# Kernel optimization log

Measured on AMD Instinct MI355X. Metric: run time of the kernel, lower is better.

Reference implementation:

```python
import jax, jax.numpy as jnp
import numpy as np

# --- cfg constants (from init_kwargs) ---
T = 100
DT_MS = 1.0
MAX_RATE_HZ = 200.0
TAU_MEM = 20.0
TAU_PRE = 20.0
TAU_POST = 20.0
V_TH = 16.0
LR_POST = 0.01
LR_PRE = 0.012
W_MAX = 1.0
B, F, N_IN = 256, 1024, 784


def setup_inputs() -> dict:
    key = jax.random.key(0)
    k1, k2, k3 = jax.random.split(key, 3)
    image = jax.random.uniform(k1, (B, 1, 28, 28), dtype=jnp.float32)
    noise = jax.random.uniform(k2, (T, B, 1, 28, 28), dtype=jnp.float32)
    # non-negative excitatory weights, kernel 28x28 flattened -> (F, 784)
    W = jax.random.uniform(k3, (F, N_IN), dtype=jnp.float32) * 0.3
    return {"image": image, "W": W, "noise": noise}


def reference(image, W, noise):
    """Returns spike_count: (B, n_filters)."""
    b = image.shape[0]
    f = W.shape[0]
    # Poisson encoding: P(spike at t) = rate*dt = image * max_rate_hz * dt_ms/1000
    p = image.reshape(b, -1) * (MAX_RATE_HZ * DT_MS / 1000.0)        # (B, 784)
    spikes_in = (noise.reshape(T, b, -1) < p[None]).astype(jnp.float32)  # (T, B, 784)

    decay_mem = jnp.float32(np.exp(-DT_MS / TAU_MEM))
    decay_pre = jnp.float32(np.exp(-DT_MS / TAU_PRE))
    decay_post = jnp.float32(np.exp(-DT_MS / TAU_POST))

    def step(carry, pre):
        mem, w, apre, apost, cnt = carry
        # conv with 28x28 kernel, padding 0 == FC: (B,784) @ (784,F)
        I = pre @ w.T                                   # (B, F)
        mem = mem * decay_mem + I
        spk = (mem >= V_TH).astype(mem.dtype)           # LIF threshold
        mem = mem * (1.0 - spk)                         # reset to 0 on spike
        # --- STDP (pair-based, batch-averaged, Diehl & Cook style) ---
        apre = apre * decay_pre + pre                   # (B, 784) pre trace
        dw_plus = (LR_POST / b) * jnp.einsum('bf,bi->fi', spk, apre)   # LTP on post spike
        dw_minus = (LR_PRE / b) * jnp.einsum('bf,bi->fi', apost, pre)  # LTD on pre spike
        w = jnp.clip(w + dw_plus - dw_minus, 0.0, W_MAX)
        apost = apost * decay_post + spk                # (B, F) post trace
        cnt = cnt + spk
        return (mem, w, apre, apost, cnt), None

    init = (jnp.zeros((b, f), jnp.float32),   # mem
            W,                                 # plastic weights
            jnp.zeros((b, N_IN), jnp.float32), # apre
            jnp.zeros((b, f), jnp.float32),    # apost
            jnp.zeros((b, f), jnp.float32))    # spike_count
    (mem, w, apre, apost, cnt), _ = jax.lax.scan(step, init, spikes_in)
    return cnt
```

## Files before the change

kernel.cpp:

```cpp
#include <hip/hip_runtime.h>
#include <math.h>

#define TSTEPS 100
#define BB 256
#define FF 1024
#define NIN 784
#define NW 13
#define CAPA 192
#define CAPB 128
#define NBLK 1024
#define TPB 256

typedef unsigned long long u64;

__device__ __forceinline__ unsigned at_add(unsigned* p, unsigned v) {
    return __hip_atomic_fetch_add(p, v, __ATOMIC_RELAXED, __HIP_MEMORY_SCOPE_AGENT);
}
__device__ __forceinline__ unsigned at_ld(unsigned* p) {
    return __hip_atomic_load(p, __ATOMIC_RELAXED, __HIP_MEMORY_SCOPE_AGENT);
}
__device__ __forceinline__ void at_st(unsigned* p, unsigned v) {
    __hip_atomic_store(p, v, __ATOMIC_RELAXED, __HIP_MEMORY_SCOPE_AGENT);
}
__device__ __forceinline__ u64 at_ld64(u64* p) {
    return __hip_atomic_load(p, __ATOMIC_RELAXED, __HIP_MEMORY_SCOPE_AGENT);
}
__device__ __forceinline__ void at_st64(u64* p, u64 v) {
    __hip_atomic_store(p, v, __ATOMIC_RELAXED, __HIP_MEMORY_SCOPE_AGENT);
}

__device__ __forceinline__ float sc0_ld(const float* p) {
    float v;
    asm volatile("global_load_dword %0, %1, off sc0\n\t"
                 "s_waitcnt vmcnt(0)"
                 : "=v"(v) : "v"(p) : "memory");
    __builtin_amdgcn_sched_barrier(0);
    return v;
}
__device__ __forceinline__ void sc0_ld2(const float* p0, const float* p1,
                                        float& v0, float& v1) {
    asm volatile("global_load_dword %0, %2, off sc0\n\t"
                 "global_load_dword %1, %3, off sc0\n\t"
                 "s_waitcnt vmcnt(0)"
                 : "=&v"(v0), "=&v"(v1) : "v"(p0), "v"(p1) : "memory");
    __builtin_amdgcn_sched_barrier(0);
}
__device__ __forceinline__ void sc0_ld8(
    const float* p0, const float* p1, const float* p2, const float* p3,
    const float* p4, const float* p5, const float* p6, const float* p7,
    float& v0, float& v1, float& v2, float& v3,
    float& v4, float& v5, float& v6, float& v7)
{
    asm volatile(
        "global_load_dword %0, %8, off sc0\n\t"
        "global_load_dword %1, %9, off sc0\n\t"
        "global_load_dword %2, %10, off sc0\n\t"
        "global_load_dword %3, %11, off sc0\n\t"
        "global_load_dword %4, %12, off sc0\n\t"
        "global_load_dword %5, %13, off sc0\n\t"
        "global_load_dword %6, %14, off sc0\n\t"
        "global_load_dword %7, %15, off sc0\n\t"
        "s_waitcnt vmcnt(0)"
        : "=&v"(v0),"=&v"(v1),"=&v"(v2),"=&v"(v3),
          "=&v"(v4),"=&v"(v5),"=&v"(v6),"=&v"(v7)
        : "v"(p0),"v"(p1),"v"(p2),"v"(p3),"v"(p4),"v"(p5),"v"(p6),"v"(p7)
        : "memory");
    __builtin_amdgcn_sched_barrier(0);
}

__global__ __launch_bounds__(256) void k_init(
    const float* __restrict__ W, float* __restrict__ wT,
    float* __restrict__ apreT_g, float* __restrict__ mem, float* __restrict__ apost,
    float* __restrict__ out, u64* __restrict__ spkbits, u64* __restrict__ spkT,
    unsigned* __restrict__ bar)
{
    int idx = blockIdx.x * 256 + threadIdx.x;
    {
        int f = idx & (FF - 1);
        int i = idx >> 10;
        wT[idx] = W[f * NIN + i];
    }
    apreT_g[idx] = 0.f;
    apreT_g[idx + NIN * FF] = 0.f;
    if (idx < BB * FF) { mem[idx] = 0.f; apost[idx] = 0.f; out[idx] = 0.f; }
    if (idx < BB * 16) spkbits[idx] = 0ull;
    if (idx < 2 * FF * 4) spkT[idx] = 0ull;
    if (idx < 4096) bar[idx] = 0u;
}

__global__ __launch_bounds__(256) void k_encode(
    const float* __restrict__ image, const float* __restrict__ noise,
    u64* __restrict__ prebits)
{
    int tid = blockIdx.x * 256 + threadIdx.x;
    int lane = threadIdx.x & 63;
    int word = tid >> 6;
    int wd = word % NW;
    int tb = word / NW;
    int b = tb & (BB - 1);
    int i = (wd << 6) + lane;
    bool s = false;
    if (i < NIN) {
        float pf = __fmul_rn(image[b * NIN + i], 0.2f);
        s = (noise[(size_t)tb * NIN + i] < pf);
    }
    u64 m = __ballot(s);
    if (lane == 0) prebits[word] = m;
}

__global__ __launch_bounds__(256) void k_encode_t(
    const u64* __restrict__ prebits, u64* __restrict__ prebitsT)
{
    int tid = blockIdx.x * 256 + threadIdx.x;
    int b = tid & (BB - 1);
    int ti = tid >> 8;
    int i = ti % NIN;
    int t = ti / NIN;
    u64 w = prebits[((size_t)t * BB + b) * NW + (i >> 6)];
    bool s = (w >> (i & 63)) & 1ull;
    u64 m = __ballot(s);
    if ((threadIdx.x & 63) == 0)
        prebitsT[(size_t)ti * 4 + ((threadIdx.x >> 6) & 3)] = m;
}

__global__ __launch_bounds__(256) void k_lists(
    const u64* __restrict__ prebits, unsigned short* __restrict__ idxA,
    unsigned short* __restrict__ cntA)
{
    int tb = blockIdx.x * 256 + threadIdx.x;
    const u64* pb = prebits + (size_t)tb * NW;
    unsigned short* ia = idxA + (size_t)tb * CAPA;
    int n = 0, c1 = 0, c2 = 0;
    for (int wd = 0; wd < NW; ++wd) {
        u64 m = pb[wd];
        int boff = wd << 6;
        while (m) {
            int j = __builtin_ctzll(m); m &= m - 1;
            if (n < CAPA) ia[n] = (unsigned short)(boff + j);
            ++n;
        }
        if (wd == 5)  c1 = n;
        if (wd == 11) c2 = n;
    }
    if (n > CAPA) n = CAPA;
    if (c2 > n) c2 = n;
    if (c1 > c2) c1 = c2;
    cntA[tb * 4 + 0] = (unsigned short)c1;
    cntA[tb * 4 + 1] = (unsigned short)c2;
    cntA[tb * 4 + 2] = (unsigned short)n;
}

__global__ __launch_bounds__(256) void k_listsT(
    const u64* __restrict__ prebitsT, unsigned char* __restrict__ idxB,
    unsigned short* __restrict__ cntB)
{
    int ti = blockIdx.x * 256 + threadIdx.x;
    if (ti >= TSTEPS * NIN) return;
    const u64* pt = prebitsT + (size_t)ti * 4;
    unsigned char* ib = idxB + (size_t)ti * CAPB;
    int n = 0;
    for (int wb = 0; wb < 4; ++wb) {
        u64 m = pt[wb];
        int boff = wb << 6;
        while (m) {
            int j = __builtin_ctzll(m); m &= m - 1;
            if (n < CAPB) ib[n] = (unsigned char)(boff + j);
            ++n;
        }
    }
    cntB[ti] = (unsigned short)(n > CAPB ? CAPB : n);
}

__global__ __launch_bounds__(TPB, 4) void k_run(
    float* __restrict__ wT, float* __restrict__ apreT_g, float* __restrict__ apost,
    float* __restrict__ mem,
    const u64* __restrict__ prebits,
    const unsigned short* __restrict__ idxA, const unsigned short* __restrict__ cntA,
    const unsigned char* __restrict__ idxB, const unsigned short* __restrict__ cntB,
    u64* __restrict__ spkbits, u64* __restrict__ spkT,
    float* __restrict__ out, unsigned* __restrict__ bar,
    float dmem, float dpre, float dpost, float lrp, float lrm)
{
    __shared__ int sh[4];
    __shared__ int shs[8];
    __shared__ float sap[2][256];
    const int tix = threadIdx.x;
    const int sub = tix >> 7, lane = tix & 127;

    if (tix == 0) {
        unsigned xcd;
        asm volatile("s_getreg_b32 %0, hwreg(HW_REG_XCC_ID)" : "=s"(xcd));
        xcd &= 7u;
        unsigned rank = at_add(bar + xcd * 16, 1u);
        asm volatile("s_waitcnt vmcnt(0)" ::: "memory");
        unsigned a = at_add(bar + 128, 1u);
        if (a == NBLK - 1u) at_st(bar + 136, 1u);
        unsigned spins = 0;
        while (at_ld(bar + 136) == 0u) {
            if (++spins > (1u << 24)) break;
            __builtin_amdgcn_s_sleep(2);
        }
        int cnts[8]; int Kn = 0, gidx = 0;
        for (int x = 0; x < 8; ++x) cnts[x] = (int)at_ld(bar + x * 16);
        for (int x = 0; x < 8; ++x)
            if (cnts[x] > 0) { if (x == (int)xcd) gidx = Kn; ++Kn; }
        int ns = 0;
        for (int s = 0; s < 8; ++s) if ((s % Kn) == gidx) shs[ns++] = s;
        sh[0] = (int)xcd; sh[1] = (int)rank; sh[2] = cnts[xcd]; sh[3] = ns;
    }
    __syncthreads();
    const int xcd = sh[0], rank = sh[1], nx = sh[2], nsl = sh[3];
    float* apx = apreT_g + (size_t)xcd * (BB * NIN);

    const int ukA = ((nsl << 8) + 2 * nx - 1) / (2 * nx);
    const int ukB = (nsl * NIN + 2 * nx - 1) / (2 * nx);
    unsigned ep = 1;

    for (int t = 0; t < TSTEPS; ++t) {
        u64* cur = spkT + (size_t)(t & 1) * (FF * 4);
        u64* nxt = spkT + (size_t)((t + 1) & 1) * (FF * 4);

        for (int q = 0; q < ukA; ++q) {
            int u = rank * 2 + sub + q * 2 * nx;
            if (u < (nsl << 8)) {
                int sl = u >> 8, b = u & 255;
                int f = (shs[sl] << 7) + lane;
                int tid = (b << 10) + f;

                u64 pw_ = spkbits[(b << 4) + (f >> 6)];
                float apo = __fadd_rn(__fmul_rn(apost[tid], dpost),
                                      (float)((pw_ >> (f & 63)) & 1ull));
                apost[tid] = apo;

                const unsigned short* ia = idxA + (size_t)(t * BB + b) * CAPA;
                const unsigned short* ca = cntA + (size_t)(t * BB + b) * 4;
                int c1 = ca[0], c2 = ca[1], c3 = ca[2];
                float I = 0.f;
                int k = 0;
                #pragma unroll 1
                for (int ch = 0; ch < 3; ++ch) {
                    int ke = (ch == 0) ? c1 : (ch == 1) ? c2 : c3;
                    float c = 0.f;
                    for (; k + 8 <= ke; k += 8) {
                        float v0,v1,v2,v3,v4,v5,v6,v7;
                        sc0_ld8(wT + ((int)ia[k+0] << 10) + f, wT + ((int)ia[k+1] << 10) + f,
                                wT + ((int)ia[k+2] << 10) + f, wT + ((int)ia[k+3] << 10) + f,
                                wT + ((int)ia[k+4] << 10) + f, wT + ((int)ia[k+5] << 10) + f,
                                wT + ((int)ia[k+6] << 10) + f, wT + ((int)ia[k+7] << 10) + f,
                                v0,v1,v2,v3,v4,v5,v6,v7);
                        c = __fadd_rn(c, v0); c = __fadd_rn(c, v1);
                        c = __fadd_rn(c, v2); c = __fadd_rn(c, v3);
                        c = __fadd_rn(c, v4); c = __fadd_rn(c, v5);
                        c = __fadd_rn(c, v6); c = __fadd_rn(c, v7);
                    }
                    for (; k < ke; ++k)
                        c = __fadd_rn(c, sc0_ld(wT + ((int)ia[k] << 10) + f));
                    I = __fadd_rn(I, c);
                }

                float mm = __fadd_rn(__fmul_rn(mem[tid], dmem), I);
                bool spk = (mm >= 16.0f);
                mem[tid] = spk ? 0.f : mm;
                if (spk) {
                    out[tid] += 1.f;
                    atomicOr(&cur[(f << 2) | (b >> 6)], 1ull << (b & 63));
                }
                u64 bal = __ballot(spk);
                if ((tix & 63) == 0) spkbits[(b << 4) + (f >> 6)] = bal;

                if (sl == 0) {
                    const u64* pbr = prebits + ((size_t)t * BB + b) * NW;
                    for (int i2 = lane; i2 < NIN; i2 += 128) {
                        u64 w_ = pbr[i2 >> 6];
                        float pr = (float)((w_ >> (i2 & 63)) & 1ull);
                        int ai = (i2 << 8) + b;
                        apx[ai] = __fadd_rn(__fmul_rn(apx[ai], dpre), pr);
                    }
                }
            }
        }
        for (int wd = rank * TPB + tix; wd < (nsl << 9); wd += nx * TPB)
            at_st64(&nxt[(shs[wd >> 9] << 9) + (wd & 511)], 0ull);

        if (t == TSTEPS - 1) break;

        asm volatile("s_waitcnt vmcnt(0) lgkmcnt(0)" ::: "memory");
        __syncthreads();
        if (tix == 0) {
            int nsub = nx < 16 ? nx : 16;
            int sb = rank % nsub;
            unsigned need = (unsigned)((nx - sb + nsub - 1) / nsub);
            unsigned v = at_add(bar + 256 + (xcd * 16 + sb) * 16, 1u);
            if (v == need * ep - 1u) {
                unsigned r = at_add(bar + 2560 + xcd * 16, 1u);
                if (r == (unsigned)nsub * ep - 1u) at_st(bar + 2816 + xcd * 16, ep);
            }
            unsigned spins = 0;
            while (at_ld(bar + 2816 + xcd * 16) < ep) {
                if (++spins > (1u << 24)) break;
                __builtin_amdgcn_s_sleep(2);
            }
        }
        __syncthreads();
        ++ep;

        for (int q = 0; q < ukB; ++q) {
            int u = rank * 2 + sub + q * 2 * nx;
            bool act = (u < nsl * NIN);
            int sl = act ? u / NIN : 0;
            int i = act ? (u - sl * NIN) : 0;
            int f = (shs[sl] << 7) + lane;
            float Sm = 0.f;
            u64 m0 = 0, m1 = 0, m2 = 0, m3 = 0;
            if (act) {
                const unsigned char* ib = idxB + (size_t)(t * NIN + i) * CAPB;
                int cb = cntB[t * NIN + i];
                int k = 0;
                for (; k + 8 <= cb; k += 8) {
                    float v0,v1,v2,v3,v4,v5,v6,v7;
                    sc0_ld8(apost + ((int)ib[k+0] << 10) + f, apost + ((int)ib[k+1] << 10) + f,
                            apost + ((int)ib[k+2] << 10) + f, apost + ((int)ib[k+3] << 10) + f,
                            apost + ((int)ib[k+4] << 10) + f, apost + ((int)ib[k+5] << 10) + f,
                            apost + ((int)ib[k+6] << 10) + f, apost + ((int)ib[k+7] << 10) + f,
                            v0,v1,v2,v3,v4,v5,v6,v7);
                    Sm = __fadd_rn(Sm, v0); Sm = __fadd_rn(Sm, v1);
                    Sm = __fadd_rn(Sm, v2); Sm = __fadd_rn(Sm, v3);
                    Sm = __fadd_rn(Sm, v4); Sm = __fadd_rn(Sm, v5);
                    Sm = __fadd_rn(Sm, v6); Sm = __fadd_rn(Sm, v7);
                }
                for (; k < cb; ++k)
                    Sm = __fadd_rn(Sm, sc0_ld(apost + ((int)ib[k] << 10) + f));

                float r0, r1;
                sc0_ld2(apx + (i << 8) + lane, apx + (i << 8) + 128 + lane, r0, r1);
                sap[sub][lane] = r0; sap[sub][128 + lane] = r1;

                m0 = at_ld64(&cur[(f << 2) | 0]);
                m1 = at_ld64(&cur[(f << 2) | 1]);
                m2 = at_ld64(&cur[(f << 2) | 2]);
                m3 = at_ld64(&cur[(f << 2) | 3]);
            }
            __syncthreads();
            if (act) {
                const float* sp_ = sap[sub];
                float Sp = 0.f;
                u64 m;
                m = m0; while (m) { int j = __builtin_ctzll(m); m &= m - 1;
                                    Sp = __fadd_rn(Sp, sp_[j]); }
                m = m1; while (m) { int j = __builtin_ctzll(m); m &= m - 1;
                                    Sp = __fadd_rn(Sp, sp_[64 + j]); }
                m = m2; while (m) { int j = __builtin_ctzll(m); m &= m - 1;
                                    Sp = __fadd_rn(Sp, sp_[128 + j]); }
                m = m3; while (m) { int j = __builtin_ctzll(m); m &= m - 1;
                                    Sp = __fadd_rn(Sp, sp_[192 + j]); }

                int wi = (i << 10) + f;
                float w = wT[wi];
                w = __fadd_rn(w, __fmul_rn(lrp, Sp));
                w = __fsub_rn(w, __fmul_rn(lrm, Sm));
                w = fminf(fmaxf(w, 0.f), 1.f);
                wT[wi] = w;
            }
            __syncthreads();
        }

        asm volatile("s_waitcnt vmcnt(0) lgkmcnt(0)" ::: "memory");
        __syncthreads();
        if (tix == 0) {
            int nsub = nx < 16 ? nx : 16;
            int sb = rank % nsub;
            unsigned need = (unsigned)((nx - sb + nsub - 1) / nsub);
            unsigned v = at_add(bar + 256 + (xcd * 16 + sb) * 16, 1u);
            if (v == need * ep - 1u) {
                unsigned r = at_add(bar + 2560 + xcd * 16, 1u);
                if (r == (unsigned)nsub * ep - 1u) at_st(bar + 2816 + xcd * 16, ep);
            }
            unsigned spins = 0;
            while (at_ld(bar + 2816 + xcd * 16) < ep) {
                if (++spins > (1u << 24)) break;
                __builtin_amdgcn_s_sleep(2);
            }
        }
        __syncthreads();
        ++ep;
    }
}

extern "C" void kernel_launch(void* const* d_in, const int* in_sizes, int n_in,
                              void* d_out, int out_size, void* d_ws, size_t ws_size,
                              hipStream_t stream)
{
    const float* image = (const float*)d_in[0];
    const float* W     = (const float*)d_in[1];
    const float* noise = (const float*)d_in[2];
    float* out = (float*)d_out;

    char* p = (char*)d_ws;
    float* wT      = (float*)p; p += (size_t)NIN * FF * 4;
    float* apreT_g = (float*)p; p += (size_t)8 * BB * NIN * 4;
    float* apost   = (float*)p; p += (size_t)BB * FF * 4;
    float* mem     = (float*)p; p += (size_t)BB * FF * 4;
    u64* prebits   = (u64*)p;   p += (size_t)TSTEPS * BB * NW * 8;
    u64* prebitsT  = (u64*)p;   p += (size_t)TSTEPS * NIN * 4 * 8;
    u64* spkbits   = (u64*)p;   p += (size_t)BB * 16 * 8;
    u64* spkT      = (u64*)p;   p += (size_t)2 * FF * 4 * 8;
    unsigned short* idxA = (unsigned short*)p; p += (size_t)TSTEPS * BB * CAPA * 2;
    unsigned short* cntA = (unsigned short*)p; p += (size_t)TSTEPS * BB * 4 * 2;
    unsigned char*  idxB = (unsigned char*)p;  p += (size_t)TSTEPS * NIN * CAPB;
    unsigned short* cntB = (unsigned short*)p; p += (size_t)TSTEPS * NIN * 2;
    unsigned* bar        = (unsigned*)p;       p += 4096 * 4;

    float dmem = (float)exp(-1.0 / 20.0);
    float dpre = dmem, dpost = dmem;
    float lrp = (float)(0.01 / 256.0);
    float lrm = (float)(0.012 / 256.0);

    k_init<<<(NIN * FF) / 256, 256, 0, stream>>>(
        W, wT, apreT_g, mem, apost, out, spkbits, spkT, bar);
    k_encode<<<(TSTEPS * BB * NW * 64) / 256, 256, 0, stream>>>(image, noise, prebits);
    k_encode_t<<<(TSTEPS * NIN * BB) / 256, 256, 0, stream>>>(prebits, prebitsT);
    k_lists<<<(TSTEPS * BB) / 256, 256, 0, stream>>>(prebits, idxA, cntA);
    k_listsT<<<(TSTEPS * NIN + 255) / 256, 256, 0, stream>>>(prebitsT, idxB, cntB);

    k_run<<<NBLK, TPB, 0, stream>>>(
        wT, apreT_g, apost, mem, prebits, idxA, cntA, idxB, cntB,
        spkbits, spkT, out, bar, dmem, dpre, dpost, lrp, lrm);
}
```

Baseline: 5.928 ms.

## Restructure persistent kernel to per-wave work units with register state and flag barrier

Reworks the persistent STDP kernel. Each wave of 64 lanes now owns a feature slice instead of each half-block of 128, membrane, count and post-trace state stay in registers across timesteps rather than round-tripping global memory, and gather loads are issued 16 at a time before a single wait. The pre-trace update is vectorized over a transposed layout, and the old atomic counter tree barrier is replaced by a per-XCD arrive/release flag barrier led by rank 0. Startup rank discovery moves to a slot table. The changes aim to cut global traffic, memory latency stalls and barrier cost, at the price of more registers per thread and more complex synchronisation.

```diff
diff --git a/kernel.cpp b/kernel.cpp
--- a/kernel.cpp
+++ b/kernel.cpp
@@ -10,12 +10,11 @@
 #define CAPB 128
 #define NBLK 1024
 #define TPB 256
+#define BARSZ 17408
 
 typedef unsigned long long u64;
-
-__device__ __forceinline__ unsigned at_add(unsigned* p, unsigned v) {
-    return __hip_atomic_fetch_add(p, v, __ATOMIC_RELAXED, __HIP_MEMORY_SCOPE_AGENT);
-}
+typedef float f4 __attribute__((ext_vector_type(4)));
+
 __device__ __forceinline__ unsigned at_ld(unsigned* p) {
     return __hip_atomic_load(p, __ATOMIC_RELAXED, __HIP_MEMORY_SCOPE_AGENT);
 }
@@ -37,15 +36,15 @@
     __builtin_amdgcn_sched_barrier(0);
     return v;
 }
-__device__ __forceinline__ void sc0_ld2(const float* p0, const float* p1,
-                                        float& v0, float& v1) {
-    asm volatile("global_load_dword %0, %2, off sc0\n\t"
-                 "global_load_dword %1, %3, off sc0\n\t"
+__device__ __forceinline__ f4 sc0_ld4(const f4* p) {
+    f4 v;
+    asm volatile("global_load_dwordx4 %0, %1, off sc0\n\t"
                  "s_waitcnt vmcnt(0)"
-                 : "=&v"(v0), "=&v"(v1) : "v"(p0), "v"(p1) : "memory");
+                 : "=v"(v) : "v"(p) : "memory");
     __builtin_amdgcn_sched_barrier(0);
-}
-__device__ __forceinline__ void sc0_ld8(
+    return v;
+}
+__device__ __forceinline__ void sc0_issue8(
     const float* p0, const float* p1, const float* p2, const float* p3,
     const float* p4, const float* p5, const float* p6, const float* p7,
     float& v0, float& v1, float& v2, float& v3,
@@ -59,19 +58,68 @@
         "global_load_dword %4, %12, off sc0\n\t"
         "global_load_dword %5, %13, off sc0\n\t"
         "global_load_dword %6, %14, off sc0\n\t"
-        "global_load_dword %7, %15, off sc0\n\t"
-        "s_waitcnt vmcnt(0)"
+        "global_load_dword %7, %15, off sc0"
         : "=&v"(v0),"=&v"(v1),"=&v"(v2),"=&v"(v3),
           "=&v"(v4),"=&v"(v5),"=&v"(v6),"=&v"(v7)
         : "v"(p0),"v"(p1),"v"(p2),"v"(p3),"v"(p4),"v"(p5),"v"(p6),"v"(p7)
         : "memory");
+}
+__device__ __forceinline__ void sc0_ld8(
+    const float* p0, const float* p1, const float* p2, const float* p3,
+    const float* p4, const float* p5, const float* p6, const float* p7,
+    float& v0, float& v1, float& v2, float& v3,
+    float& v4, float& v5, float& v6, float& v7)
+{
+    sc0_issue8(p0,p1,p2,p3,p4,p5,p6,p7, v0,v1,v2,v3,v4,v5,v6,v7);
+    asm volatile("s_waitcnt vmcnt(0)" ::: "memory");
     __builtin_amdgcn_sched_barrier(0);
+}
+
+template <typename IDX>
+__device__ __forceinline__ float foldList(
+    const float* __restrict__ base, const IDX* __restrict__ list,
+    int k0, int k1, int f)
+{
+    float c = 0.f;
+    int k = k0;
+    for (; k + 16 <= k1; k += 16) {
+        float v0,v1,v2,v3,v4,v5,v6,v7,v8,v9,v10,v11,v12,v13,v14,v15;
+        sc0_issue8(base+((int)list[k+0]<<10)+f, base+((int)list[k+1]<<10)+f,
+                   base+((int)list[k+2]<<10)+f, base+((int)list[k+3]<<10)+f,
+                   base+((int)list[k+4]<<10)+f, base+((int)list[k+5]<<10)+f,
+                   base+((int)list[k+6]<<10)+f, base+((int)list[k+7]<<10)+f,
+                   v0,v1,v2,v3,v4,v5,v6,v7);
+        sc0_issue8(base+((int)list[k+8]<<10)+f,  base+((int)list[k+9]<<10)+f,
+                   base+((int)list[k+10]<<10)+f, base+((int)list[k+11]<<10)+f,
+                   base+((int)list[k+12]<<10)+f, base+((int)list[k+13]<<10)+f,
+                   base+((int)list[k+14]<<10)+f, base+((int)list[k+15]<<10)+f,
+                   v8,v9,v10,v11,v12,v13,v14,v15);
+        asm volatile("s_waitcnt vmcnt(0)" ::: "memory");
+        __builtin_amdgcn_sched_barrier(0);
+        c=__fadd_rn(c,v0);  c=__fadd_rn(c,v1);  c=__fadd_rn(c,v2);  c=__fadd_rn(c,v3);
+        c=__fadd_rn(c,v4);  c=__fadd_rn(c,v5);  c=__fadd_rn(c,v6);  c=__fadd_rn(c,v7);
+        c=__fadd_rn(c,v8);  c=__fadd_rn(c,v9);  c=__fadd_rn(c,v10); c=__fadd_rn(c,v11);
+        c=__fadd_rn(c,v12); c=__fadd_rn(c,v13); c=__fadd_rn(c,v14); c=__fadd_rn(c,v15);
+    }
+    if (k + 8 <= k1) {
+        float v0,v1,v2,v3,v4,v5,v6,v7;
+        sc0_ld8(base+((int)list[k+0]<<10)+f, base+((int)list[k+1]<<10)+f,
+                base+((int)list[k+2]<<10)+f, base+((int)list[k+3]<<10)+f,
+                base+((int)list[k+4]<<10)+f, base+((int)list[k+5]<<10)+f,
+                base+((int)list[k+6]<<10)+f, base+((int)list[k+7]<<10)+f,
+                v0,v1,v2,v3,v4,v5,v6,v7);
+        c=__fadd_rn(c,v0); c=__fadd_rn(c,v1); c=__fadd_rn(c,v2); c=__fadd_rn(c,v3);
+        c=__fadd_rn(c,v4); c=__fadd_rn(c,v5); c=__fadd_rn(c,v6); c=__fadd_rn(c,v7);
+        k += 8;
+    }
+    for (; k < k1; ++k)
+        c = __fadd_rn(c, sc0_ld(base + ((int)list[k] << 10) + f));
+    return c;
 }
 
 __global__ __launch_bounds__(256) void k_init(
     const float* __restrict__ W, float* __restrict__ wT,
-    float* __restrict__ apreT_g, float* __restrict__ mem, float* __restrict__ apost,
-    float* __restrict__ out, u64* __restrict__ spkbits, u64* __restrict__ spkT,
+    float* __restrict__ apreT_g, u64* __restrict__ spkT,
     unsigned* __restrict__ bar)
 {
     int idx = blockIdx.x * 256 + threadIdx.x;
@@ -82,10 +130,8 @@
     }
     apreT_g[idx] = 0.f;
     apreT_g[idx + NIN * FF] = 0.f;
-    if (idx < BB * FF) { mem[idx] = 0.f; apost[idx] = 0.f; out[idx] = 0.f; }
-    if (idx < BB * 16) spkbits[idx] = 0ull;
     if (idx < 2 * FF * 4) spkT[idx] = 0ull;
-    if (idx < 4096) bar[idx] = 0u;
+    if (idx < BARSZ) bar[idx] = 0u;
 }
 
 __global__ __launch_bounds__(256) void k_encode(
@@ -173,217 +219,228 @@
 
 __global__ __launch_bounds__(TPB, 4) void k_run(
     float* __restrict__ wT, float* __restrict__ apreT_g, float* __restrict__ apost,
-    float* __restrict__ mem,
-    const u64* __restrict__ prebits,
     const unsigned short* __restrict__ idxA, const unsigned short* __restrict__ cntA,
     const unsigned char* __restrict__ idxB, const unsigned short* __restrict__ cntB,
-    u64* __restrict__ spkbits, u64* __restrict__ spkT,
+    const u64* __restrict__ prebitsT, u64* __restrict__ spkT,
     float* __restrict__ out, unsigned* __restrict__ bar,
     float dmem, float dpre, float dpost, float lrp, float lrm)
 {
-    __shared__ int sh[4];
-    __shared__ int shs[8];
-    __shared__ float sap[2][256];
+    __shared__ int shs[16];
+    __shared__ int shinfo[4];
+    __shared__ unsigned scnt[9];
+    __shared__ int sbad;
+    __shared__ float sap[4][256];
+
     const int tix = threadIdx.x;
-    const int sub = tix >> 7, lane = tix & 127;
-
+    const int wv = tix >> 6, lane = tix & 63;
+    const int bid = blockIdx.x;
+
+    unsigned* slot = bar;
+    if (tix < 9) scnt[tix] = 0u;
     if (tix == 0) {
-        unsigned xcd;
-        asm volatile("s_getreg_b32 %0, hwreg(HW_REG_XCC_ID)" : "=s"(xcd));
-        xcd &= 7u;
-        unsigned rank = at_add(bar + xcd * 16, 1u);
-        asm volatile("s_waitcnt vmcnt(0)" ::: "memory");
-        unsigned a = at_add(bar + 128, 1u);
-        if (a == NBLK - 1u) at_st(bar + 136, 1u);
-        unsigned spins = 0;
-        while (at_ld(bar + 136) == 0u) {
-            if (++spins > (1u << 24)) break;
-            __builtin_amdgcn_s_sleep(2);
-        }
-        int cnts[8]; int Kn = 0, gidx = 0;
-        for (int x = 0; x < 8; ++x) cnts[x] = (int)at_ld(bar + x * 16);
-        for (int x = 0; x < 8; ++x)
-            if (cnts[x] > 0) { if (x == (int)xcd) gidx = Kn; ++Kn; }
-        int ns = 0;
-        for (int s = 0; s < 8; ++s) if ((s % Kn) == gidx) shs[ns++] = s;
-        sh[0] = (int)xcd; sh[1] = (int)rank; sh[2] = cnts[xcd]; sh[3] = ns;
+        unsigned x;
+        asm volatile("s_getreg_b32 %0, hwreg(HW_REG_XCC_ID)" : "=s"(x));
+        shinfo[0] = (int)(x & 7u);
+        at_st(&slot[bid], (x & 7u) + 1u);
     }
     __syncthreads();
-    const int xcd = sh[0], rank = sh[1], nx = sh[2], nsl = sh[3];
+    const int xcd = shinfo[0];
+    unsigned mv0, mv1, mv2, mv3;
+    for (int rounds = 0;; ++rounds) {
+        if (tix == 0) sbad = 0;
+        __syncthreads();
+        mv0 = at_ld(&slot[tix]);
+        mv1 = at_ld(&slot[256 + tix]);
+        mv2 = at_ld(&slot[512 + tix]);
+        mv3 = at_ld(&slot[768 + tix]);
+        if (!(mv0 && mv1 && mv2 && mv3)) sbad = 1;
+        __syncthreads();
+        if (!sbad || rounds > (1 << 20)) break;
+        __builtin_amdgcn_s_sleep(2);
+    }
+    {
+        atomicAdd(&scnt[mv0 - 1u], 1u);
+        atomicAdd(&scnt[mv1 - 1u], 1u);
+        atomicAdd(&scnt[mv2 - 1u], 1u);
+        atomicAdd(&scnt[mv3 - 1u], 1u);
+        unsigned r = 0;
+        if ((int)(mv0 - 1u) == xcd && tix < bid) r++;
+        if ((int)(mv1 - 1u) == xcd && 256 + tix < bid) r++;
+        if ((int)(mv2 - 1u) == xcd && 512 + tix < bid) r++;
+        if ((int)(mv3 - 1u) == xcd && 768 + tix < bid) r++;
+        if (r) atomicAdd(&scnt[8], r);
+        __syncthreads();
+        if (tix == 0) {
+            int Kn = 0, gidx = 0;
+            for (int x2 = 0; x2 < 8; ++x2)
+                if (scnt[x2] > 0) { if (x2 == xcd) gidx = Kn; ++Kn; }
+            int ns = 0;
+            for (int s = 0; s < 16; ++s)
+                if ((s % Kn) == gidx) shs[ns++] = s;
+            shinfo[1] = (int)scnt[8];
+            shinfo[2] = (int)scnt[xcd];
+            shinfo[3] = ns;
+        }
+        __syncthreads();
+    }
+    const int rank = shinfo[1], nx = shinfo[2], nsl = shinfo[3];
+    const int nxw = nx * 4;
+    const int wrank = rank * 4 + wv;
+    const int nA = nsl << 8;
+    const int nB = nsl * NIN;
     float* apx = apreT_g + (size_t)xcd * (BB * NIN);
-
-    const int ukA = ((nsl << 8) + 2 * nx - 1) / (2 * nx);
-    const int ukB = (nsl * NIN + 2 * nx - 1) / (2 * nx);
+    float* sapw = sap[wv];
+    unsigned* arrive  = bar + 1024 + xcd * 1024;
+    unsigned* release = bar + 9216 + xcd * 1024;
     unsigned ep = 1;
+
+#define A_STATE(Q) float memv##Q = 0.f, cntv##Q = 0.f, apov##Q = 0.f; u64 pbal##Q = 0ull;
+    A_STATE(0) A_STATE(1) A_STATE(2) A_STATE(3)
+
+#define DO_A(Q) do { \
+    int u = wrank + (Q) * nxw; \
+    if (u < nA) { \
+        int sl = u >> 8, b = u & 255; \
+        int f = (shs[sl] << 6) + lane; \
+        apov##Q = __fadd_rn(__fmul_rn(apov##Q, dpost), \
+                            (float)((pbal##Q >> lane) & 1ull)); \
+        apost[(b << 10) + f] = apov##Q; \
+        const unsigned short* ia = idxA + (size_t)(t * BB + b) * CAPA; \
+        const unsigned short* ca = cntA + (size_t)(t * BB + b) * 4; \
+        int c1 = ca[0], c2 = ca[1], c3 = ca[2]; \
+        float I = 0.f; \
+        I = __fadd_rn(I, foldList(wT, ia, 0,  c1, f)); \
+        I = __fadd_rn(I, foldList(wT, ia, c1, c2, f)); \
+        I = __fadd_rn(I, foldList(wT, ia, c2, c3, f)); \
+        float mm = __fadd_rn(__fmul_rn(memv##Q, dmem), I); \
+        bool spk = (mm >= 16.0f); \
+        memv##Q = spk ? 0.f : mm; \
+        if (spk) { \
+            cntv##Q += 1.f; \
+            atomicOr(&cur[(f << 2) | (b >> 6)], 1ull << (b & 63)); \
+        } \
+        pbal##Q = __ballot(spk); \
+    } \
+} while (0)
+
+    auto xbar = [&]() {
+        asm volatile("s_waitcnt vmcnt(0) lgkmcnt(0)" ::: "memory");
+        __syncthreads();
+        if (rank == 0) {
+            for (int rounds = 0;; ++rounds) {
+                if (tix == 0) sbad = 0;
+                __syncthreads();
+                bool ok = true;
+                #pragma unroll
+                for (int kk = 0; kk < 4; ++kk) {
+                    int r = kk * 256 + tix;
+                    if (r < nx && r > 0) ok &= (at_ld(&arrive[r]) >= ep);
+                }
+                if (!ok) sbad = 1;
+                __syncthreads();
+                if (!sbad || rounds > (1 << 20)) break;
+                __builtin_amdgcn_s_sleep(4);
+            }
+            #pragma unroll
+            for (int kk = 0; kk < 4; ++kk) {
+                int r = kk * 256 + tix;
+                if (r < nx) at_st(&release[r], ep);
+            }
+        } else {
+            if (tix == 0) {
+                at_st(&arrive[rank], ep);
+                unsigned spins = 0;
+                while (at_ld(&release[rank]) < ep) {
+                    if (++spins > (1u << 22)) break;
+                    __builtin_amdgcn_s_sleep(8);
+                }
+            }
+            __syncthreads();
+        }
+        ++ep;
+    };
 
     for (int t = 0; t < TSTEPS; ++t) {
         u64* cur = spkT + (size_t)(t & 1) * (FF * 4);
         u64* nxt = spkT + (size_t)((t + 1) & 1) * (FF * 4);
 
-        for (int q = 0; q < ukA; ++q) {
-            int u = rank * 2 + sub + q * 2 * nx;
-            if (u < (nsl << 8)) {
-                int sl = u >> 8, b = u & 255;
-                int f = (shs[sl] << 7) + lane;
-                int tid = (b << 10) + f;
-
-                u64 pw_ = spkbits[(b << 4) + (f >> 6)];
-                float apo = __fadd_rn(__fmul_rn(apost[tid], dpost),
-                                      (float)((pw_ >> (f & 63)) & 1ull));
-                apost[tid] = apo;
-
-                const unsigned short* ia = idxA + (size_t)(t * BB + b) * CAPA;
-                const unsigned short* ca = cntA + (size_t)(t * BB + b) * 4;
-                int c1 = ca[0], c2 = ca[1], c3 = ca[2];
-                float I = 0.f;
-                int k = 0;
-                #pragma unroll 1
-                for (int ch = 0; ch < 3; ++ch) {
-                    int ke = (ch == 0) ? c1 : (ch == 1) ? c2 : c3;
-                    float c = 0.f;
-                    for (; k + 8 <= ke; k += 8) {
-                        float v0,v1,v2,v3,v4,v5,v6,v7;
-                        sc0_ld8(wT + ((int)ia[k+0] << 10) + f, wT + ((int)ia[k+1] << 10) + f,
-                                wT + ((int)ia[k+2] << 10) + f, wT + ((int)ia[k+3] << 10) + f,
-                                wT + ((int)ia[k+4] << 10) + f, wT + ((int)ia[k+5] << 10) + f,
-                                wT + ((int)ia[k+6] << 10) + f, wT + ((int)ia[k+7] << 10) + f,
-                                v0,v1,v2,v3,v4,v5,v6,v7);
-                        c = __fadd_rn(c, v0); c = __fadd_rn(c, v1);
-                        c = __fadd_rn(c, v2); c = __fadd_rn(c, v3);
-                        c = __fadd_rn(c, v4); c = __fadd_rn(c, v5);
-                        c = __fadd_rn(c, v6); c = __fadd_rn(c, v7);
-                    }
-                    for (; k < ke; ++k)
-                        c = __fadd_rn(c, sc0_ld(wT + ((int)ia[k] << 10) + f));
-                    I = __fadd_rn(I, c);
-                }
-
-                float mm = __fadd_rn(__fmul_rn(mem[tid], dmem), I);
-                bool spk = (mm >= 16.0f);
-                mem[tid] = spk ? 0.f : mm;
-                if (spk) {
-                    out[tid] += 1.f;
-                    atomicOr(&cur[(f << 2) | (b >> 6)], 1ull << (b & 63));
-                }
-                u64 bal = __ballot(spk);
-                if ((tix & 63) == 0) spkbits[(b << 4) + (f >> 6)] = bal;
-
-                if (sl == 0) {
-                    const u64* pbr = prebits + ((size_t)t * BB + b) * NW;
-                    for (int i2 = lane; i2 < NIN; i2 += 128) {
-                        u64 w_ = pbr[i2 >> 6];
-                        float pr = (float)((w_ >> (i2 & 63)) & 1ull);
-                        int ai = (i2 << 8) + b;
-                        apx[ai] = __fadd_rn(__fmul_rn(apx[ai], dpre), pr);
-                    }
-                }
-            }
-        }
-        for (int wd = rank * TPB + tix; wd < (nsl << 9); wd += nx * TPB)
-            at_st64(&nxt[(shs[wd >> 9] << 9) + (wd & 511)], 0ull);
+        DO_A(0); DO_A(1); DO_A(2); DO_A(3);
+
+        for (int r = wrank; r < NIN; r += nxw) {
+            const u64* pt = prebitsT + ((size_t)t * NIN + r) * 4;
+            u64 w0 = pt[0], w1 = pt[1], w2 = pt[2], w3 = pt[3];
+            int bb = lane << 2;
+            u64 wsel = (bb & 128) ? ((bb & 64) ? w3 : w2)
+                                  : ((bb & 64) ? w1 : w0);
+            int s0 = bb & 63;
+            f4* vp = (f4*)(apx + ((size_t)r << 8) + bb);
+            f4 v = *vp;
+            v.x = __fadd_rn(__fmul_rn(v.x, dpre), (float)((wsel >> s0) & 1ull));
+            v.y = __fadd_rn(__fmul_rn(v.y, dpre), (float)((wsel >> (s0+1)) & 1ull));
+            v.z = __fadd_rn(__fmul_rn(v.z, dpre), (float)((wsel >> (s0+2)) & 1ull));
+            v.w = __fadd_rn(__fmul_rn(v.w, dpre), (float)((wsel >> (s0+3)) & 1ull));
+            *vp = v;
+        }
+        for (int wd0 = rank * TPB + tix; wd0 < (nsl << 8); wd0 += nx * TPB) {
+            int sl = wd0 >> 8, rest = wd0 & 255;
+            int f = (shs[sl] << 6) + (rest >> 2);
+            at_st64(&nxt[(f << 2) + (rest & 3)], 0ull);
+        }
 
         if (t == TSTEPS - 1) break;
-
-        asm volatile("s_waitcnt vmcnt(0) lgkmcnt(0)" ::: "memory");
-        __syncthreads();
-        if (tix == 0) {
-            int nsub = nx < 16 ? nx : 16;
-            int sb = rank % nsub;
-            unsigned need = (unsigned)((nx - sb + nsub - 1) / nsub);
-            unsigned v = at_add(bar + 256 + (xcd * 16 + sb) * 16, 1u);
-            if (v == need * ep - 1u) {
-                unsigned r = at_add(bar + 2560 + xcd * 16, 1u);
-                if (r == (unsigned)nsub * ep - 1u) at_st(bar + 2816 + xcd * 16, ep);
-            }
-            unsigned spins = 0;
-            while (at_ld(bar + 2816 + xcd * 16) < ep) {
-                if (++spins > (1u << 24)) break;
-                __builtin_amdgcn_s_sleep(2);
-            }
-        }
-        __syncthreads();
-        ++ep;
-
-        for (int q = 0; q < ukB; ++q) {
-            int u = rank * 2 + sub + q * 2 * nx;
-            bool act = (u < nsl * NIN);
-            int sl = act ? u / NIN : 0;
-            int i = act ? (u - sl * NIN) : 0;
-            int f = (shs[sl] << 7) + lane;
-            float Sm = 0.f;
-            u64 m0 = 0, m1 = 0, m2 = 0, m3 = 0;
-            if (act) {
-                const unsigned char* ib = idxB + (size_t)(t * NIN + i) * CAPB;
-                int cb = cntB[t * NIN + i];
-                int k = 0;
-                for (; k + 8 <= cb; k += 8) {
-                    float v0,v1,v2,v3,v4,v5,v6,v7;
-                    sc0_ld8(apost + ((int)ib[k+0] << 10) + f, apost + ((int)ib[k+1] << 10) + f,
-                            apost + ((int)ib[k+2] << 10) + f, apost + ((int)ib[k+3] << 10) + f,
-                            apost + ((int)ib[k+4] << 10) + f, apost + ((int)ib[k+5] << 10) + f,
-                            apost + ((int)ib[k+6] << 10) + f, apost + ((int)ib[k+7] << 10) + f,
-                            v0,v1,v2,v3,v4,v5,v6,v7);
-                    Sm = __fadd_rn(Sm, v0); Sm = __fadd_rn(Sm, v1);
-                    Sm = __fadd_rn(Sm, v2); Sm = __fadd_rn(Sm, v3);
-                    Sm = __fadd_rn(Sm, v4); Sm = __fadd_rn(Sm, v5);
-                    Sm = __fadd_rn(Sm, v6); Sm = __fadd_rn(Sm, v7);
-                }
-                for (; k < cb; ++k)
-                    Sm = __fadd_rn(Sm, sc0_ld(apost + ((int)ib[k] << 10) + f));
-
-                float r0, r1;
-                sc0_ld2(apx + (i << 8) + lane, apx + (i << 8) + 128 + lane, r0, r1);
-                sap[sub][lane] = r0; sap[sub][128 + lane] = r1;
-
-                m0 = at_ld64(&cur[(f << 2) | 0]);
-                m1 = at_ld64(&cur[(f << 2) | 1]);
-                m2 = at_ld64(&cur[(f << 2) | 2]);
-                m3 = at_ld64(&cur[(f << 2) | 3]);
-            }
-            __syncthreads();
-            if (act) {
-                const float* sp_ = sap[sub];
-                float Sp = 0.f;
-                u64 m;
-                m = m0; while (m) { int j = __builtin_ctzll(m); m &= m - 1;
-                                    Sp = __fadd_rn(Sp, sp_[j]); }
-                m = m1; while (m) { int j = __builtin_ctzll(m); m &= m - 1;
-                                    Sp = __fadd_rn(Sp, sp_[64 + j]); }
-                m = m2; while (m) { int j = __builtin_ctzll(m); m &= m - 1;
-                                    Sp = __fadd_rn(Sp, sp_[128 + j]); }
-                m = m3; while (m) { int j = __builtin_ctzll(m); m &= m - 1;
-                                    Sp = __fadd_rn(Sp, sp_[192 + j]); }
-
-                int wi = (i << 10) + f;
-                float w = wT[wi];
-                w = __fadd_rn(w, __fmul_rn(lrp, Sp));
-                w = __fsub_rn(w, __fmul_rn(lrm, Sm));
-                w = fminf(fmaxf(w, 0.f), 1.f);
-                wT[wi] = w;
-            }
-            __syncthreads();
-        }
-
-        asm volatile("s_waitcnt vmcnt(0) lgkmcnt(0)" ::: "memory");
-        __syncthreads();
-        if (tix == 0) {
-            int nsub = nx < 16 ? nx : 16;
-            int sb = rank % nsub;
-            unsigned need = (unsigned)((nx - sb + nsub - 1) / nsub);
-            unsigned v = at_add(bar + 256 + (xcd * 16 + sb) * 16, 1u);
-            if (v == need * ep - 1u) {
-                unsigned r = at_add(bar + 2560 + xcd * 16, 1u);
-                if (r == (unsigned)nsub * ep - 1u) at_st(bar + 2816 + xcd * 16, ep);
-            }
-            unsigned spins = 0;
-            while (at_ld(bar + 2816 + xcd * 16) < ep) {
-                if (++spins > (1u << 24)) break;
-                __builtin_amdgcn_s_sleep(2);
-            }
-        }
-        __syncthreads();
-        ++ep;
-    }
+        xbar();
+
+        for (int q = 0;; ++q) {
+            int u = wrank + q * nxw;
+            if (u >= nB) break;
+            int sl = u / NIN, i = u - sl * NIN;
+            int f = (shs[sl] << 6) + lane;
+
+            const unsigned char* ib = idxB + (size_t)(t * NIN + i) * CAPB;
+            int cb = cntB[t * NIN + i];
+            float Sm = foldList(apost, ib, 0, cb, f);
+
+            asm volatile("s_waitcnt lgkmcnt(0)" ::: "memory");
+            __builtin_amdgcn_sched_barrier(0);
+            f4 rv = sc0_ld4((const f4*)(apx + ((size_t)i << 8) + (lane << 2)));
+            *(f4*)(sapw + (lane << 2)) = rv;
+            u64 m0 = at_ld64(&cur[(f << 2) | 0]);
+            u64 m1 = at_ld64(&cur[(f << 2) | 1]);
+            u64 m2 = at_ld64(&cur[(f << 2) | 2]);
+            u64 m3 = at_ld64(&cur[(f << 2) | 3]);
+            asm volatile("s_waitcnt lgkmcnt(0)" ::: "memory");
+            __builtin_amdgcn_sched_barrier(0);
+
+            float Sp = 0.f;
+            u64 m;
+            m = m0; while (m) { int j = __builtin_ctzll(m); m &= m - 1;
+                                Sp = __fadd_rn(Sp, sapw[j]); }
+            m = m1; while (m) { int j = __builtin_ctzll(m); m &= m - 1;
+                                Sp = __fadd_rn(Sp, sapw[64 + j]); }
+            m = m2; while (m) { int j = __builtin_ctzll(m); m &= m - 1;
+                                Sp = __fadd_rn(Sp, sapw[128 + j]); }
+            m = m3; while (m) { int j = __builtin_ctzll(m); m &= m - 1;
+                                Sp = __fadd_rn(Sp, sapw[192 + j]); }
+
+            int wi = (i << 10) + f;
+            float w = wT[wi];
+            w = __fadd_rn(w, __fmul_rn(lrp, Sp));
+            w = __fsub_rn(w, __fmul_rn(lrm, Sm));
+            w = fminf(fmaxf(w, 0.f), 1.f);
+            wT[wi] = w;
+        }
+        xbar();
+    }
+
+#define DO_OUT(Q) do { \
+    int u = wrank + (Q) * nxw; \
+    if (u < nA) { \
+        int sl = u >> 8, b = u & 255; \
+        int f = (shs[sl] << 6) + lane; \
+        out[(b << 10) + f] = cntv##Q; \
+    } \
+} while (0)
+    DO_OUT(0); DO_OUT(1); DO_OUT(2); DO_OUT(3);
 }
 
 extern "C" void kernel_launch(void* const* d_in, const int* in_sizes, int n_in,
@@ -399,30 +456,27 @@
     float* wT      = (float*)p; p += (size_t)NIN * FF * 4;
     float* apreT_g = (float*)p; p += (size_t)8 * BB * NIN * 4;
     float* apost   = (float*)p; p += (size_t)BB * FF * 4;
-    float* mem     = (float*)p; p += (size_t)BB * FF * 4;
     u64* prebits   = (u64*)p;   p += (size_t)TSTEPS * BB * NW * 8;
     u64* prebitsT  = (u64*)p;   p += (size_t)TSTEPS * NIN * 4 * 8;
-    u64* spkbits   = (u64*)p;   p += (size_t)BB * 16 * 8;
     u64* spkT      = (u64*)p;   p += (size_t)2 * FF * 4 * 8;
     unsigned short* idxA = (unsigned short*)p; p += (size_t)TSTEPS * BB * CAPA * 2;
     unsigned short* cntA = (unsigned short*)p; p += (size_t)TSTEPS * BB * 4 * 2;
     unsigned char*  idxB = (unsigned char*)p;  p += (size_t)TSTEPS * NIN * CAPB;
     unsigned short* cntB = (unsigned short*)p; p += (size_t)TSTEPS * NIN * 2;
-    unsigned* bar        = (unsigned*)p;       p += 4096 * 4;
+    unsigned* bar        = (unsigned*)p;       p += (size_t)BARSZ * 4;
 
     float dmem = (float)exp(-1.0 / 20.0);
     float dpre = dmem, dpost = dmem;
     float lrp = (float)(0.01 / 256.0);
     float lrm = (float)(0.012 / 256.0);
 
-    k_init<<<(NIN * FF) / 256, 256, 0, stream>>>(
-        W, wT, apreT_g, mem, apost, out, spkbits, spkT, bar);
+    k_init<<<(NIN * FF) / 256, 256, 0, stream>>>(W, wT, apreT_g, spkT, bar);
     k_encode<<<(TSTEPS * BB * NW * 64) / 256, 256, 0, stream>>>(image, noise, prebits);
     k_encode_t<<<(TSTEPS * NIN * BB) / 256, 256, 0, stream>>>(prebits, prebitsT);
     k_lists<<<(TSTEPS * BB) / 256, 256, 0, stream>>>(prebits, idxA, cntA);
     k_listsT<<<(TSTEPS * NIN + 255) / 256, 256, 0, stream>>>(prebitsT, idxB, cntB);
 
     k_run<<<NBLK, TPB, 0, stream>>>(
-        wT, apreT_g, apost, mem, prebits, idxA, cntA, idxB, cntB,
-        spkbits, spkT, out, bar, dmem, dpre, dpost, lrp, lrm);
-}
+        wT, apreT_g, apost, idxA, cntA, idxB, cntB,
+        prebitsT, spkT, out, bar, dmem, dpre, dpost, lrp, lrm);
+}
```

New measurement: 4.842 ms. 18.3% less time.
